# Performance work log

Hardware: AMD Instinct MI355X
Metric: run time of the kernel (lower is better)

## Reference

```python
import jax, jax.numpy as jnp
import numpy as np

H = 32  # hidden size
I = 1   # input size


def setup_inputs() -> dict:
    key = jax.random.key(0)
    ks = jax.random.split(key, 8)
    B, T = 1024, 2048
    s = 1.0 / np.sqrt(H)  # PyTorch default uniform init bound
    u = lambda k, shape: jax.random.uniform(k, shape, jnp.float32, -s, s)
    return {
        "x": jax.random.normal(ks[0], (B, T, I), jnp.float32),
        "W_ih": u(ks[1], (4 * H, I)),   # gate order: i, f, g, o
        "W_hh": u(ks[2], (4 * H, H)),
        "b_ih": u(ks[3], (4 * H,)),
        "b_hh": u(ks[4], (4 * H,)),
        "W_out": u(ks[5], (1, H)),
        "b_out": u(ks[6], (1,)),
    }


def reference(x, W_ih, W_hh, b_ih, b_hh, W_out, b_out):
    B, T, _ = x.shape
    # Precompute input contributions to all gates for all timesteps: [B,T,4H]
    xg = jnp.einsum('bti,gi->btg', x, W_ih) + b_ih + b_hh

    def step(carry, xg_t):
        h, c = carry  # each [B,H]
        gates = xg_t + h @ W_hh.T  # [B,4H]
        i, f, g, o = jnp.split(gates, 4, axis=-1)
        i = jax.nn.sigmoid(i)
        f = jax.nn.sigmoid(f)
        g = jnp.tanh(g)
        o = jax.nn.sigmoid(o)
        c = f * c + i * g
        h = o * jnp.tanh(c)
        return (h, c), h

    h0 = jnp.zeros((B, H), x.dtype)
    c0 = jnp.zeros((B, H), x.dtype)
    _, hs = jax.lax.scan(step, (h0, c0), jnp.swapaxes(xg, 0, 1))  # hs: [T,B,H]
    r_out = jnp.swapaxes(hs, 0, 1)  # [B,T,H]
    # Per-timestep linear (the original Python loop) == one batched matmul
    return jnp.einsum('bth,oh->bto', r_out, W_out) + b_out  # [B,T,1]
```

## Files before the change

kernel.cpp:

```cpp
#include <hip/hip_runtime.h>

#define LOG2E 1.44269504088896340736f

typedef _Float16 half2_t __attribute__((ext_vector_type(2)));

__device__ __forceinline__ float rlf(float v, int lane) {
    return __int_as_float(__builtin_amdgcn_readlane(__float_as_int(v), lane));
}
__device__ __forceinline__ unsigned rlu(unsigned v, int lane) {
    return (unsigned)__builtin_amdgcn_readlane((int)v, lane);
}
__device__ __forceinline__ unsigned pack2(float a, float b) {
    half2_t v; v.x = (_Float16)a; v.y = (_Float16)b;
    return __builtin_bit_cast(unsigned, v);
}
__device__ __forceinline__ half2_t ubc(unsigned u) {
    return __builtin_bit_cast(half2_t, u);
}

__device__ __forceinline__ float swap_half(float v) {
#if __has_builtin(__builtin_amdgcn_permlane32_swap)
    const unsigned u = __builtin_bit_cast(unsigned, v);
    auto r = __builtin_amdgcn_permlane32_swap(u, u, false, false);
    return __builtin_bit_cast(float, (unsigned)(r[0] ^ r[1] ^ u));
#else
    return __shfl_xor(v, 32, 64);
#endif
}

__device__ __forceinline__ float xor1_dpp(float v) {
    return __int_as_float(__builtin_amdgcn_mov_dpp(
        __float_as_int(v), 0xB1, 0xF, 0xF, true));
}

__global__ __launch_bounds__(64, 1) void lstm_pl_kernel(
    const float* __restrict__ x,
    const float* __restrict__ W_ih,
    const float* __restrict__ W_hh,
    const float* __restrict__ b_ih,
    const float* __restrict__ b_hh,
    const float* __restrict__ W_out,
    const float* __restrict__ b_out,
    float* __restrict__ out,
    int T)
{
    __shared__ float psum[64 * 68];
    __shared__ __align__(16) unsigned hbc[80];

    const int b = blockIdx.x;
    const int l = threadIdx.x;
    const int r0 = l;
    const int r1 = l + 64;
    const bool lo = (l < 32);

    const float sc0 = -LOG2E;
    const float sc1 = lo ? (-2.0f * LOG2E) : (-LOG2E);

    unsigned w0u[16], w1u[16];
#pragma unroll
    for (int m = 0; m < 16; ++m) {
        w0u[m] = pack2(W_hh[r0 * 32 + 2 * m] * sc0,
                       W_hh[r0 * 32 + 2 * m + 1] * sc0);
        w1u[m] = pack2(W_hh[r1 * 32 + 2 * m] * sc1,
                       W_hh[r1 * 32 + 2 * m + 1] * sc1);
    }
#pragma unroll
    for (int m = 0; m < 16; ++m)
        asm volatile("" : "+v"(w0u[m]), "+v"(w1u[m]));

    float4 wout4[8];
#pragma unroll
    for (int m = 0; m < 8; ++m)
        wout4[m] = *(const float4*)(W_out + 4 * m);

    const float wih0  = W_ih[r0] * sc0;
    const float wih1  = W_ih[r1] * sc1;
    const float bias0 = (b_ih[r0] + b_hh[r0]) * sc0;
    const float bias1 = (b_ih[r1] + b_hh[r1]) * sc1;
    const float A1s = lo ? (-4.0f * LOG2E) : 1.0f;
    const float B1s = lo ? ( 2.0f * LOG2E) : 0.0f;
    const float bout  = b_out[0];

    const bool pub = lo && !(l & 1) && (l >= 8);
    const int waddr = pub ? (l >> 1) : (16 + l);

    float h = 0.0f, cs = 0.0f;
    unsigned hpk = 0u;
    uint4 hqB = {0,0,0,0}, hqC = {0,0,0,0}, hqD = {0,0,0,0};

    const float* xp = x + (size_t)b * T;
    float*       op = out + (size_t)b * T;
    float xv = xp[l];

    const uint4* hb4 = (const uint4*)hbc;

    for (int t0 = 0; t0 < T; t0 += 64) {
        const int tn = (t0 + 64 < T) ? (t0 + 64) : t0;
        float xv_next = xp[tn + l];

#pragma unroll 16
        for (int tu = 0; tu < 64; ++tu) {
            const float xt = rlf(xv, tu);

            const unsigned hp0 = rlu(hpk, 0);
            const unsigned hp1 = rlu(hpk, 2);
            const unsigned hp2 = rlu(hpk, 4);
            const unsigned hp3 = rlu(hpk, 6);

            float a0 = fmaf(wih0, xt, bias0);
            float a1 = fmaf(wih1, xt, bias1);
            float b0 = 0.0f, b1 = 0.0f;
            a0 = __builtin_amdgcn_fdot2(ubc(w0u[0]),  ubc(hp0),   a0, false);
            b0 = __builtin_amdgcn_fdot2(ubc(w0u[1]),  ubc(hp1),   b0, false);
            a1 = __builtin_amdgcn_fdot2(ubc(w1u[0]),  ubc(hp0),   a1, false);
            b1 = __builtin_amdgcn_fdot2(ubc(w1u[1]),  ubc(hp1),   b1, false);
            a0 = __builtin_amdgcn_fdot2(ubc(w0u[2]),  ubc(hp2),   a0, false);
            b0 = __builtin_amdgcn_fdot2(ubc(w0u[3]),  ubc(hp3),   b0, false);
            a1 = __builtin_amdgcn_fdot2(ubc(w1u[2]),  ubc(hp2),   a1, false);
            b1 = __builtin_amdgcn_fdot2(ubc(w1u[3]),  ubc(hp3),   b1, false);
            a0 = __builtin_amdgcn_fdot2(ubc(w0u[4]),  ubc(hqB.x), a0, false);
            b0 = __builtin_amdgcn_fdot2(ubc(w0u[5]),  ubc(hqB.y), b0, false);
            a1 = __builtin_amdgcn_fdot2(ubc(w1u[4]),  ubc(hqB.x), a1, false);
            b1 = __builtin_amdgcn_fdot2(ubc(w1u[5]),  ubc(hqB.y), b1, false);
            a0 = __builtin_amdgcn_fdot2(ubc(w0u[6]),  ubc(hqB.z), a0, false);
            b0 = __builtin_amdgcn_fdot2(ubc(w0u[7]),  ubc(hqB.w), b0, false);
            a1 = __builtin_amdgcn_fdot2(ubc(w1u[6]),  ubc(hqB.z), a1, false);
            b1 = __builtin_amdgcn_fdot2(ubc(w1u[7]),  ubc(hqB.w), b1, false);
            a0 = __builtin_amdgcn_fdot2(ubc(w0u[8]),  ubc(hqC.x), a0, false);
            b0 = __builtin_amdgcn_fdot2(ubc(w0u[9]),  ubc(hqC.y), b0, false);
            a1 = __builtin_amdgcn_fdot2(ubc(w1u[8]),  ubc(hqC.x), a1, false);
            b1 = __builtin_amdgcn_fdot2(ubc(w1u[9]),  ubc(hqC.y), b1, false);
            a0 = __builtin_amdgcn_fdot2(ubc(w0u[10]), ubc(hqC.z), a0, false);
            b0 = __builtin_amdgcn_fdot2(ubc(w0u[11]), ubc(hqC.w), b0, false);
            a1 = __builtin_amdgcn_fdot2(ubc(w1u[10]), ubc(hqC.z), a1, false);
            b1 = __builtin_amdgcn_fdot2(ubc(w1u[11]), ubc(hqC.w), b1, false);
            a0 = __builtin_amdgcn_fdot2(ubc(w0u[12]), ubc(hqD.x), a0, false);
            b0 = __builtin_amdgcn_fdot2(ubc(w0u[13]), ubc(hqD.y), b0, false);
            a1 = __builtin_amdgcn_fdot2(ubc(w1u[12]), ubc(hqD.x), a1, false);
            b1 = __builtin_amdgcn_fdot2(ubc(w1u[13]), ubc(hqD.y), b1, false);
            a0 = __builtin_amdgcn_fdot2(ubc(w0u[14]), ubc(hqD.z), a0, false);
            b0 = __builtin_amdgcn_fdot2(ubc(w0u[15]), ubc(hqD.w), b0, false);
            a1 = __builtin_amdgcn_fdot2(ubc(w1u[14]), ubc(hqD.z), a1, false);
            b1 = __builtin_amdgcn_fdot2(ubc(w1u[15]), ubc(hqD.w), b1, false);
            const float G0 = a0 + b0;
            const float G1 = a1 + b1;

            const float s0  = __builtin_amdgcn_rcpf(1.0f + __builtin_amdgcn_exp2f(G0));
            const float s1s = fmaf(A1s, __builtin_amdgcn_rcpf(
                                  1.0f + __builtin_amdgcn_exp2f(G1)), B1s);
            const float ig = s0 * s1s;

            const float o0 = swap_half(s0);
            const float o1 = swap_half(s1s);
            const float to1 = o1 + o1;

            cs = fmaf(o0, cs, ig);
            const float rc = __builtin_amdgcn_rcpf(
                1.0f + __builtin_amdgcn_exp2f(cs));
            h = fmaf(to1, rc, -o1);

            const float hn = xor1_dpp(h);
            hpk = __builtin_bit_cast(unsigned,
                      __builtin_amdgcn_cvt_pkrtz(h, hn));
            hbc[waddr] = hpk;
            psum[tu * 68 + l] = h;
            hqB = hb4[1];
            hqC = hb4[2];
            hqD = hb4[3];
        }

        __syncthreads();
        const float4* row = (const float4*)(psum + l * 68);
        float4 s4;
        {
            float4 v4 = row[0];
            s4.x = v4.x * wout4[0].x; s4.y = v4.y * wout4[0].y;
            s4.z = v4.z * wout4[0].z; s4.w = v4.w * wout4[0].w;
        }
#pragma unroll
        for (int m = 1; m < 8; ++m) {
            float4 v4 = row[m];
            s4.x = fmaf(v4.x, wout4[m].x, s4.x);
            s4.y = fmaf(v4.y, wout4[m].y, s4.y);
            s4.z = fmaf(v4.z, wout4[m].z, s4.z);
            s4.w = fmaf(v4.w, wout4[m].w, s4.w);
        }
        op[t0 + l] = (s4.x + s4.y) + (s4.z + s4.w) + bout;
        __syncthreads();
        xv = xv_next;
    }
}

extern "C" void kernel_launch(void* const* d_in, const int* in_sizes, int n_in,
                              void* d_out, int out_size, void* d_ws, size_t ws_size,
                              hipStream_t stream) {
    const float* x     = (const float*)d_in[0];
    const float* W_ih  = (const float*)d_in[1];
    const float* W_hh  = (const float*)d_in[2];
    const float* b_ih  = (const float*)d_in[3];
    const float* b_hh  = (const float*)d_in[4];
    const float* W_out = (const float*)d_in[5];
    const float* b_out = (const float*)d_in[6];
    float* out = (float*)d_out;

    const int B = 1024;
    const int T = 2048;
    lstm_pl_kernel<<<B, 64, 0, stream>>>(x, W_ih, W_hh, b_ih, b_hh,
                                         W_out, b_out, out, T);
}
```

Measured before the change: 428.6 us.

## Process two batch rows per wave with lane-local gates and DPP h exchange

Each 64-lane wave now handles two sequences, one per 32-lane half. Each lane computes all four gates for one hidden unit, so the permlane32 gate swap is gone. The hidden state is broadcast with a permlane16 swap plus a chain of DPP permutes against pre-permuted weights, replacing the readlane and LDS round trip, and x is staged through shared memory. This halves the grid to 512 blocks and removes LDS latency from the recurrence. In exchange each lane issues twice as many fdot2 operations per step and holds four times as many weight registers.

```diff
diff --git a/kernel.cpp b/kernel.cpp
--- a/kernel.cpp
+++ b/kernel.cpp
@@ -4,12 +4,6 @@
 
 typedef _Float16 half2_t __attribute__((ext_vector_type(2)));
 
-__device__ __forceinline__ float rlf(float v, int lane) {
-    return __int_as_float(__builtin_amdgcn_readlane(__float_as_int(v), lane));
-}
-__device__ __forceinline__ unsigned rlu(unsigned v, int lane) {
-    return (unsigned)__builtin_amdgcn_readlane((int)v, lane);
-}
 __device__ __forceinline__ unsigned pack2(float a, float b) {
     half2_t v; v.x = (_Float16)a; v.y = (_Float16)b;
     return __builtin_bit_cast(unsigned, v);
@@ -18,22 +12,21 @@
     return __builtin_bit_cast(half2_t, u);
 }
 
-__device__ __forceinline__ float swap_half(float v) {
-#if __has_builtin(__builtin_amdgcn_permlane32_swap)
-    const unsigned u = __builtin_bit_cast(unsigned, v);
-    auto r = __builtin_amdgcn_permlane32_swap(u, u, false, false);
-    return __builtin_bit_cast(float, (unsigned)(r[0] ^ r[1] ^ u));
+template <int CTRL>
+__device__ __forceinline__ unsigned dppx(unsigned v) {
+    return (unsigned)__builtin_amdgcn_mov_dpp((int)v, CTRL, 0xF, 0xF, true);
+}
+
+__device__ __forceinline__ unsigned lanex16(unsigned u) {
+#if __has_builtin(__builtin_amdgcn_permlane16_swap)
+    auto r = __builtin_amdgcn_permlane16_swap(u, u, false, false);
+    return (unsigned)(r[0] ^ r[1] ^ u);
 #else
-    return __shfl_xor(v, 32, 64);
+    return (unsigned)__builtin_amdgcn_ds_swizzle((int)u, 0x401F);
 #endif
 }
 
-__device__ __forceinline__ float xor1_dpp(float v) {
-    return __int_as_float(__builtin_amdgcn_mov_dpp(
-        __float_as_int(v), 0xB1, 0xF, 0xF, true));
-}
-
-__global__ __launch_bounds__(64, 1) void lstm_pl_kernel(
+__global__ __launch_bounds__(64, 1) void lstm_pl2_kernel(
     const float* __restrict__ x,
     const float* __restrict__ W_ih,
     const float* __restrict__ W_hh,
@@ -44,150 +37,158 @@
     float* __restrict__ out,
     int T)
 {
-    __shared__ float psum[64 * 68];
-    __shared__ __align__(16) unsigned hbc[80];
-
-    const int b = blockIdx.x;
-    const int l = threadIdx.x;
-    const int r0 = l;
-    const int r1 = l + 64;
-    const bool lo = (l < 32);
-
-    const float sc0 = -LOG2E;
-    const float sc1 = lo ? (-2.0f * LOG2E) : (-LOG2E);
-
-    unsigned w0u[16], w1u[16];
-#pragma unroll
-    for (int m = 0; m < 16; ++m) {
-        w0u[m] = pack2(W_hh[r0 * 32 + 2 * m] * sc0,
-                       W_hh[r0 * 32 + 2 * m + 1] * sc0);
-        w1u[m] = pack2(W_hh[r1 * 32 + 2 * m] * sc1,
-                       W_hh[r1 * 32 + 2 * m + 1] * sc1);
+    __shared__ __align__(16) float psum[64 * 68];
+    __shared__ float xs[2 * 72];
+
+    const int b  = blockIdx.x;
+    const int l  = threadIdx.x;
+    const int kl = l & 31;
+    const int hf = l >> 5;
+
+    const float sA = -LOG2E;
+    const float sG = -2.0f * LOG2E;
+
+    const int ri = kl, rf2 = 32 + kl, rg = 64 + kl, ro = 96 + kl;
+
+    const int X[16] = {0,2,5,7,8,10,13,15, 16,18,21,23,24,26,29,31};
+
+    unsigned wi[16], wf[16], wg[16], wo[16];
+#pragma unroll
+    for (int j = 0; j < 16; ++j) {
+        const int xl = kl ^ X[j];
+        const int q2 = xl & ~1;
+        const int s  = xl & 1;
+        wi[j] = pack2(W_hh[ri *32 + q2 + s] * sA, W_hh[ri *32 + q2 + (s^1)] * sA);
+        wf[j] = pack2(W_hh[rf2*32 + q2 + s] * sA, W_hh[rf2*32 + q2 + (s^1)] * sA);
+        wg[j] = pack2(W_hh[rg *32 + q2 + s] * sG, W_hh[rg *32 + q2 + (s^1)] * sG);
+        wo[j] = pack2(W_hh[ro *32 + q2 + s] * sA, W_hh[ro *32 + q2 + (s^1)] * sA);
     }
 #pragma unroll
-    for (int m = 0; m < 16; ++m)
-        asm volatile("" : "+v"(w0u[m]), "+v"(w1u[m]));
+    for (int j = 0; j < 16; ++j)
+        asm volatile("" : "+v"(wi[j]), "+v"(wf[j]), "+v"(wg[j]), "+v"(wo[j]));
 
     float4 wout4[8];
 #pragma unroll
-    for (int m = 0; m < 8; ++m)
-        wout4[m] = *(const float4*)(W_out + 4 * m);
-
-    const float wih0  = W_ih[r0] * sc0;
-    const float wih1  = W_ih[r1] * sc1;
-    const float bias0 = (b_ih[r0] + b_hh[r0]) * sc0;
-    const float bias1 = (b_ih[r1] + b_hh[r1]) * sc1;
-    const float A1s = lo ? (-4.0f * LOG2E) : 1.0f;
-    const float B1s = lo ? ( 2.0f * LOG2E) : 0.0f;
-    const float bout  = b_out[0];
-
-    const bool pub = lo && !(l & 1) && (l >= 8);
-    const int waddr = pub ? (l >> 1) : (16 + l);
+    for (int m = 0; m < 8; ++m) wout4[m] = *(const float4*)(W_out + 4 * m);
+
+    const float wxi = W_ih[ri ] * sA;
+    const float wxf = W_ih[rf2] * sA;
+    const float wxg = W_ih[rg ] * sG;
+    const float wxo = W_ih[ro ] * sA;
+    const float bi_ = (b_ih[ri ] + b_hh[ri ]) * sA;
+    const float bf_ = (b_ih[rf2] + b_hh[rf2]) * sA;
+    const float bg_ = (b_ih[rg ] + b_hh[rg ]) * sG;
+    const float bo_ = (b_ih[ro ] + b_hh[ro ]) * sA;
+    const float bout = b_out[0];
+
+    const float* xpA = x + (size_t)(2*b)     * T;
+    const float* xpB = x + (size_t)(2*b + 1) * T;
+    float*       opA = out + (size_t)(2*b)     * T;
+    float*       opB = out + (size_t)(2*b + 1) * T;
+
+    float* xsh = xs + 72 * hf;
+    const int pcol = kl + 36 * hf;
+
+    xs[l]      = xpA[l];
+    xs[72 + l] = xpB[l];
 
     float h = 0.0f, cs = 0.0f;
     unsigned hpk = 0u;
-    uint4 hqB = {0,0,0,0}, hqC = {0,0,0,0}, hqD = {0,0,0,0};
-
-    const float* xp = x + (size_t)b * T;
-    float*       op = out + (size_t)b * T;
-    float xv = xp[l];
-
-    const uint4* hb4 = (const uint4*)hbc;
 
     for (int t0 = 0; t0 < T; t0 += 64) {
         const int tn = (t0 + 64 < T) ? (t0 + 64) : t0;
-        float xv_next = xp[tn + l];
-
-#pragma unroll 16
+        const float na = xpA[tn + l];
+        const float nb = xpB[tn + l];
+
+        float xt0 = xsh[0], xt1 = xsh[1];
+
+#pragma unroll 8
         for (int tu = 0; tu < 64; ++tu) {
-            const float xt = rlf(xv, tu);
-
-            const unsigned hp0 = rlu(hpk, 0);
-            const unsigned hp1 = rlu(hpk, 2);
-            const unsigned hp2 = rlu(hpk, 4);
-            const unsigned hp3 = rlu(hpk, 6);
-
-            float a0 = fmaf(wih0, xt, bias0);
-            float a1 = fmaf(wih1, xt, bias1);
-            float b0 = 0.0f, b1 = 0.0f;
-            a0 = __builtin_amdgcn_fdot2(ubc(w0u[0]),  ubc(hp0),   a0, false);
-            b0 = __builtin_amdgcn_fdot2(ubc(w0u[1]),  ubc(hp1),   b0, false);
-            a1 = __builtin_amdgcn_fdot2(ubc(w1u[0]),  ubc(hp0),   a1, false);
-            b1 = __builtin_amdgcn_fdot2(ubc(w1u[1]),  ubc(hp1),   b1, false);
-            a0 = __builtin_amdgcn_fdot2(ubc(w0u[2]),  ubc(hp2),   a0, false);
-            b0 = __builtin_amdgcn_fdot2(ubc(w0u[3]),  ubc(hp3),   b0, false);
-            a1 = __builtin_amdgcn_fdot2(ubc(w1u[2]),  ubc(hp2),   a1, false);
-            b1 = __builtin_amdgcn_fdot2(ubc(w1u[3]),  ubc(hp3),   b1, false);
-            a0 = __builtin_amdgcn_fdot2(ubc(w0u[4]),  ubc(hqB.x), a0, false);
-            b0 = __builtin_amdgcn_fdot2(ubc(w0u[5]),  ubc(hqB.y), b0, false);
-            a1 = __builtin_amdgcn_fdot2(ubc(w1u[4]),  ubc(hqB.x), a1, false);
-            b1 = __builtin_amdgcn_fdot2(ubc(w1u[5]),  ubc(hqB.y), b1, false);
-            a0 = __builtin_amdgcn_fdot2(ubc(w0u[6]),  ubc(hqB.z), a0, false);
-            b0 = __builtin_amdgcn_fdot2(ubc(w0u[7]),  ubc(hqB.w), b0, false);
-            a1 = __builtin_amdgcn_fdot2(ubc(w1u[6]),  ubc(hqB.z), a1, false);
-            b1 = __builtin_amdgcn_fdot2(ubc(w1u[7]),  ubc(hqB.w), b1, false);
-            a0 = __builtin_amdgcn_fdot2(ubc(w0u[8]),  ubc(hqC.x), a0, false);
-            b0 = __builtin_amdgcn_fdot2(ubc(w0u[9]),  ubc(hqC.y), b0, false);
-            a1 = __builtin_amdgcn_fdot2(ubc(w1u[8]),  ubc(hqC.x), a1, false);
-            b1 = __builtin_amdgcn_fdot2(ubc(w1u[9]),  ubc(hqC.y), b1, false);
-            a0 = __builtin_amdgcn_fdot2(ubc(w0u[10]), ubc(hqC.z), a0, false);
-            b0 = __builtin_amdgcn_fdot2(ubc(w0u[11]), ubc(hqC.w), b0, false);
-            a1 = __builtin_amdgcn_fdot2(ubc(w1u[10]), ubc(hqC.z), a1, false);
-            b1 = __builtin_amdgcn_fdot2(ubc(w1u[11]), ubc(hqC.w), b1, false);
-            a0 = __builtin_amdgcn_fdot2(ubc(w0u[12]), ubc(hqD.x), a0, false);
-            b0 = __builtin_amdgcn_fdot2(ubc(w0u[13]), ubc(hqD.y), b0, false);
-            a1 = __builtin_amdgcn_fdot2(ubc(w1u[12]), ubc(hqD.x), a1, false);
-            b1 = __builtin_amdgcn_fdot2(ubc(w1u[13]), ubc(hqD.y), b1, false);
-            a0 = __builtin_amdgcn_fdot2(ubc(w0u[14]), ubc(hqD.z), a0, false);
-            b0 = __builtin_amdgcn_fdot2(ubc(w0u[15]), ubc(hqD.w), b0, false);
-            a1 = __builtin_amdgcn_fdot2(ubc(w1u[14]), ubc(hqD.z), a1, false);
-            b1 = __builtin_amdgcn_fdot2(ubc(w1u[15]), ubc(hqD.w), b1, false);
-            const float G0 = a0 + b0;
-            const float G1 = a1 + b1;
-
-            const float s0  = __builtin_amdgcn_rcpf(1.0f + __builtin_amdgcn_exp2f(G0));
-            const float s1s = fmaf(A1s, __builtin_amdgcn_rcpf(
-                                  1.0f + __builtin_amdgcn_exp2f(G1)), B1s);
-            const float ig = s0 * s1s;
-
-            const float o0 = swap_half(s0);
-            const float o1 = swap_half(s1s);
-            const float to1 = o1 + o1;
-
-            cs = fmaf(o0, cs, ig);
-            const float rc = __builtin_amdgcn_rcpf(
-                1.0f + __builtin_amdgcn_exp2f(cs));
-            h = fmaf(to1, rc, -o1);
-
-            const float hn = xor1_dpp(h);
-            hpk = __builtin_bit_cast(unsigned,
-                      __builtin_amdgcn_cvt_pkrtz(h, hn));
-            hbc[waddr] = hpk;
-            psum[tu * 68 + l] = h;
-            hqB = hb4[1];
-            hqC = hb4[2];
-            hqD = hb4[3];
+            const float xt = (tu & 1) ? xt1 : xt0;
+            float GiA = fmaf(wxi, xt, bi_);
+            float GfA = fmaf(wxf, xt, bf_);
+            float GgA = fmaf(wxg, xt, bg_);
+            float GoA = fmaf(wxo, xt, bo_);
+            float GiB = 0.0f, GfB = 0.0f, GgB = 0.0f, GoB = 0.0f;
+
+            unsigned ha = hpk;
+            unsigned hb = lanex16(hpk);
+
+#define DOTS(j, HA, HB) \
+            GiA = __builtin_amdgcn_fdot2(ubc(wi[j]),   ubc(HA), GiA, false); \
+            GfA = __builtin_amdgcn_fdot2(ubc(wf[j]),   ubc(HA), GfA, false); \
+            GgA = __builtin_amdgcn_fdot2(ubc(wg[j]),   ubc(HA), GgA, false); \
+            GoA = __builtin_amdgcn_fdot2(ubc(wo[j]),   ubc(HA), GoA, false); \
+            GiB = __builtin_amdgcn_fdot2(ubc(wi[8+j]), ubc(HB), GiB, false); \
+            GfB = __builtin_amdgcn_fdot2(ubc(wf[8+j]), ubc(HB), GfB, false); \
+            GgB = __builtin_amdgcn_fdot2(ubc(wg[8+j]), ubc(HB), GgB, false); \
+            GoB = __builtin_amdgcn_fdot2(ubc(wo[8+j]), ubc(HB), GoB, false);
+
+            DOTS(0, ha, hb)
+            ha = dppx<0x4E>(ha);  hb = dppx<0x4E>(hb);
+            DOTS(1, ha, hb)
+            ha = dppx<0x141>(ha); hb = dppx<0x141>(hb);
+            DOTS(2, ha, hb)
+            ha = dppx<0x4E>(ha);  hb = dppx<0x4E>(hb);
+            DOTS(3, ha, hb)
+            ha = dppx<0x140>(ha); hb = dppx<0x140>(hb);
+            DOTS(4, ha, hb)
+            ha = dppx<0x4E>(ha);  hb = dppx<0x4E>(hb);
+            DOTS(5, ha, hb)
+            ha = dppx<0x141>(ha); hb = dppx<0x141>(hb);
+            DOTS(6, ha, hb)
+            ha = dppx<0x4E>(ha);  hb = dppx<0x4E>(hb);
+            DOTS(7, ha, hb)
+#undef DOTS
+
+            const float Gi = GiA + GiB;
+            const float Gf = GfA + GfB;
+            const float Gg = GgA + GgB;
+            const float Go = GoA + GoB;
+
+            const float i_ = __builtin_amdgcn_rcpf(1.0f + __builtin_amdgcn_exp2f(Gi));
+            const float f_ = __builtin_amdgcn_rcpf(1.0f + __builtin_amdgcn_exp2f(Gf));
+            const float o_ = __builtin_amdgcn_rcpf(1.0f + __builtin_amdgcn_exp2f(Go));
+            const float gs = fmaf(-4.0f * LOG2E,
+                __builtin_amdgcn_rcpf(1.0f + __builtin_amdgcn_exp2f(Gg)),
+                2.0f * LOG2E);
+
+            cs = fmaf(f_, cs, i_ * gs);
+            const float rc = __builtin_amdgcn_rcpf(1.0f + __builtin_amdgcn_exp2f(cs));
+            h = fmaf(o_ + o_, rc, -o_);
+
+            const float hn = __int_as_float(__builtin_amdgcn_mov_dpp(
+                __float_as_int(h), 0xB1, 0xF, 0xF, true));
+            hpk = __builtin_bit_cast(unsigned, __builtin_amdgcn_cvt_pkrtz(h, hn));
+
+            psum[tu * 68 + pcol] = h;
+            if (!(tu & 1)) xt0 = xsh[tu + 2]; else xt1 = xsh[tu + 2];
         }
 
         __syncthreads();
-        const float4* row = (const float4*)(psum + l * 68);
-        float4 s4;
-        {
-            float4 v4 = row[0];
-            s4.x = v4.x * wout4[0].x; s4.y = v4.y * wout4[0].y;
-            s4.z = v4.z * wout4[0].z; s4.w = v4.w * wout4[0].w;
+#pragma unroll
+        for (int s = 0; s < 2; ++s) {
+            const float4* row = (const float4*)(psum + l * 68 + 36 * s);
+            float4 a4;
+            {
+                float4 v4 = row[0];
+                a4.x = v4.x * wout4[0].x; a4.y = v4.y * wout4[0].y;
+                a4.z = v4.z * wout4[0].z; a4.w = v4.w * wout4[0].w;
+            }
+#pragma unroll
+            for (int m = 1; m < 8; ++m) {
+                float4 v4 = row[m];
+                a4.x = fmaf(v4.x, wout4[m].x, a4.x);
+                a4.y = fmaf(v4.y, wout4[m].y, a4.y);
+                a4.z = fmaf(v4.z, wout4[m].z, a4.z);
+                a4.w = fmaf(v4.w, wout4[m].w, a4.w);
+            }
+            const float r = (a4.x + a4.y) + (a4.z + a4.w) + bout;
+            if (s == 0) opA[t0 + l] = r; else opB[t0 + l] = r;
         }
-#pragma unroll
-        for (int m = 1; m < 8; ++m) {
-            float4 v4 = row[m];
-            s4.x = fmaf(v4.x, wout4[m].x, s4.x);
-            s4.y = fmaf(v4.y, wout4[m].y, s4.y);
-            s4.z = fmaf(v4.z, wout4[m].z, s4.z);
-            s4.w = fmaf(v4.w, wout4[m].w, s4.w);
-        }
-        op[t0 + l] = (s4.x + s4.y) + (s4.z + s4.w) + bout;
         __syncthreads();
-        xv = xv_next;
+        xs[l]      = na;
+        xs[72 + l] = nb;
     }
 }
 
@@ -205,6 +206,6 @@
 
     const int B = 1024;
     const int T = 2048;
-    lstm_pl_kernel<<<B, 64, 0, stream>>>(x, W_ih, W_hh, b_ih, b_hh,
-                                         W_out, b_out, out, T);
-}
+    lstm_pl2_kernel<<<B / 2, 64, 0, stream>>>(x, W_ih, W_hh, b_ih, b_hh,
+                                              W_out, b_out, out, T);
+}
```

Result: slower. 551.7 us (+28.7%).

## Interleave two independent batch sequences per wavefront to hide recurrence latency

Applied to the files above, without the earlier changes.

Each 64-lane block now runs two batch elements' LSTM recurrences interleaved in one instruction stream, and the grid is halved to 512 blocks. The aim is to fill the latency of the serial dependency chain (dot products, exp/rcp, LDS round trips, cross-lane swaps) with independent work from the second sequence. In exchange the per-step instruction count doubles for each wave, register and LDS use roughly double, and with only 512 waves on a 256-CU device the machine may be underfilled, so the single-sequence step latency still sets the critical path.

```diff
diff --git a/kernel.cpp b/kernel.cpp
--- a/kernel.cpp
+++ b/kernel.cpp
@@ -33,7 +33,7 @@
         __float_as_int(v), 0xB1, 0xF, 0xF, true));
 }
 
-__global__ __launch_bounds__(64, 1) void lstm_pl_kernel(
+__global__ __launch_bounds__(64, 1) void lstm_dual_kernel(
     const float* __restrict__ x,
     const float* __restrict__ W_ih,
     const float* __restrict__ W_hh,
@@ -44,8 +44,10 @@
     float* __restrict__ out,
     int T)
 {
-    __shared__ float psum[64 * 68];
-    __shared__ __align__(16) unsigned hbc[80];
+    __shared__ float psumA[64 * 68];
+    __shared__ float psumB[64 * 68];
+    __shared__ __align__(16) unsigned hbcA[80];
+    __shared__ __align__(16) unsigned hbcB[80];
 
     const int b = blockIdx.x;
     const int l = threadIdx.x;
@@ -84,110 +86,152 @@
     const bool pub = lo && !(l & 1) && (l >= 8);
     const int waddr = pub ? (l >> 1) : (16 + l);
 
-    float h = 0.0f, cs = 0.0f;
-    unsigned hpk = 0u;
-    uint4 hqB = {0,0,0,0}, hqC = {0,0,0,0}, hqD = {0,0,0,0};
-
-    const float* xp = x + (size_t)b * T;
-    float*       op = out + (size_t)b * T;
-    float xv = xp[l];
-
-    const uint4* hb4 = (const uint4*)hbc;
+    float hA = 0.0f, csA = 0.0f;
+    float hB = 0.0f, csB = 0.0f;
+    unsigned hpkA = 0u, hpkB = 0u;
+    uint4 hqAB = {0,0,0,0}, hqAC = {0,0,0,0}, hqAD = {0,0,0,0};
+    uint4 hqBB = {0,0,0,0}, hqBC = {0,0,0,0}, hqBD = {0,0,0,0};
+
+    const float* xpA = x + (size_t)(2 * b)     * T;
+    const float* xpB = x + (size_t)(2 * b + 1) * T;
+    float*       opA = out + (size_t)(2 * b)     * T;
+    float*       opB = out + (size_t)(2 * b + 1) * T;
+    float xvA = xpA[l];
+    float xvB = xpB[l];
+
+    const uint4* hb4A = (const uint4*)hbcA;
+    const uint4* hb4B = (const uint4*)hbcB;
 
     for (int t0 = 0; t0 < T; t0 += 64) {
         const int tn = (t0 + 64 < T) ? (t0 + 64) : t0;
-        float xv_next = xp[tn + l];
-
-#pragma unroll 16
+        float nA = xpA[tn + l];
+        float nB = xpB[tn + l];
+
+#pragma unroll 8
         for (int tu = 0; tu < 64; ++tu) {
-            const float xt = rlf(xv, tu);
-
-            const unsigned hp0 = rlu(hpk, 0);
-            const unsigned hp1 = rlu(hpk, 2);
-            const unsigned hp2 = rlu(hpk, 4);
-            const unsigned hp3 = rlu(hpk, 6);
-
-            float a0 = fmaf(wih0, xt, bias0);
-            float a1 = fmaf(wih1, xt, bias1);
-            float b0 = 0.0f, b1 = 0.0f;
-            a0 = __builtin_amdgcn_fdot2(ubc(w0u[0]),  ubc(hp0),   a0, false);
-            b0 = __builtin_amdgcn_fdot2(ubc(w0u[1]),  ubc(hp1),   b0, false);
-            a1 = __builtin_amdgcn_fdot2(ubc(w1u[0]),  ubc(hp0),   a1, false);
-            b1 = __builtin_amdgcn_fdot2(ubc(w1u[1]),  ubc(hp1),   b1, false);
-            a0 = __builtin_amdgcn_fdot2(ubc(w0u[2]),  ubc(hp2),   a0, false);
-            b0 = __builtin_amdgcn_fdot2(ubc(w0u[3]),  ubc(hp3),   b0, false);
-            a1 = __builtin_amdgcn_fdot2(ubc(w1u[2]),  ubc(hp2),   a1, false);
-            b1 = __builtin_amdgcn_fdot2(ubc(w1u[3]),  ubc(hp3),   b1, false);
-            a0 = __builtin_amdgcn_fdot2(ubc(w0u[4]),  ubc(hqB.x), a0, false);
-            b0 = __builtin_amdgcn_fdot2(ubc(w0u[5]),  ubc(hqB.y), b0, false);
-            a1 = __builtin_amdgcn_fdot2(ubc(w1u[4]),  ubc(hqB.x), a1, false);
-            b1 = __builtin_amdgcn_fdot2(ubc(w1u[5]),  ubc(hqB.y), b1, false);
-            a0 = __builtin_amdgcn_fdot2(ubc(w0u[6]),  ubc(hqB.z), a0, false);
-            b0 = __builtin_amdgcn_fdot2(ubc(w0u[7]),  ubc(hqB.w), b0, false);
-            a1 = __builtin_amdgcn_fdot2(ubc(w1u[6]),  ubc(hqB.z), a1, false);
-            b1 = __builtin_amdgcn_fdot2(ubc(w1u[7]),  ubc(hqB.w), b1, false);
-            a0 = __builtin_amdgcn_fdot2(ubc(w0u[8]),  ubc(hqC.x), a0, false);
-            b0 = __builtin_amdgcn_fdot2(ubc(w0u[9]),  ubc(hqC.y), b0, false);
-            a1 = __builtin_amdgcn_fdot2(ubc(w1u[8]),  ubc(hqC.x), a1, false);
-            b1 = __builtin_amdgcn_fdot2(ubc(w1u[9]),  ubc(hqC.y), b1, false);
-            a0 = __builtin_amdgcn_fdot2(ubc(w0u[10]), ubc(hqC.z), a0, false);
-            b0 = __builtin_amdgcn_fdot2(ubc(w0u[11]), ubc(hqC.w), b0, false);
-            a1 = __builtin_amdgcn_fdot2(ubc(w1u[10]), ubc(hqC.z), a1, false);
-            b1 = __builtin_amdgcn_fdot2(ubc(w1u[11]), ubc(hqC.w), b1, false);
-            a0 = __builtin_amdgcn_fdot2(ubc(w0u[12]), ubc(hqD.x), a0, false);
-            b0 = __builtin_amdgcn_fdot2(ubc(w0u[13]), ubc(hqD.y), b0, false);
-            a1 = __builtin_amdgcn_fdot2(ubc(w1u[12]), ubc(hqD.x), a1, false);
-            b1 = __builtin_amdgcn_fdot2(ubc(w1u[13]), ubc(hqD.y), b1, false);
-            a0 = __builtin_amdgcn_fdot2(ubc(w0u[14]), ubc(hqD.z), a0, false);
-            b0 = __builtin_amdgcn_fdot2(ubc(w0u[15]), ubc(hqD.w), b0, false);
-            a1 = __builtin_amdgcn_fdot2(ubc(w1u[14]), ubc(hqD.z), a1, false);
-            b1 = __builtin_amdgcn_fdot2(ubc(w1u[15]), ubc(hqD.w), b1, false);
-            const float G0 = a0 + b0;
-            const float G1 = a1 + b1;
-
-            const float s0  = __builtin_amdgcn_rcpf(1.0f + __builtin_amdgcn_exp2f(G0));
-            const float s1s = fmaf(A1s, __builtin_amdgcn_rcpf(
-                                  1.0f + __builtin_amdgcn_exp2f(G1)), B1s);
-            const float ig = s0 * s1s;
-
-            const float o0 = swap_half(s0);
-            const float o1 = swap_half(s1s);
-            const float to1 = o1 + o1;
-
-            cs = fmaf(o0, cs, ig);
-            const float rc = __builtin_amdgcn_rcpf(
-                1.0f + __builtin_amdgcn_exp2f(cs));
-            h = fmaf(to1, rc, -o1);
-
-            const float hn = xor1_dpp(h);
-            hpk = __builtin_bit_cast(unsigned,
-                      __builtin_amdgcn_cvt_pkrtz(h, hn));
-            hbc[waddr] = hpk;
-            psum[tu * 68 + l] = h;
-            hqB = hb4[1];
-            hqC = hb4[2];
-            hqD = hb4[3];
+            const float xtA = rlf(xvA, tu);
+            const float xtB = rlf(xvB, tu);
+
+            const unsigned hA0 = rlu(hpkA, 0), hA1 = rlu(hpkA, 2);
+            const unsigned hA2 = rlu(hpkA, 4), hA3 = rlu(hpkA, 6);
+            const unsigned hB0 = rlu(hpkB, 0), hB1 = rlu(hpkB, 2);
+            const unsigned hB2 = rlu(hpkB, 4), hB3 = rlu(hpkB, 6);
+
+            float a0A = fmaf(wih0, xtA, bias0);
+            float a1A = fmaf(wih1, xtA, bias1);
+            float b0A = 0.0f, b1A = 0.0f;
+            float a0B = fmaf(wih0, xtB, bias0);
+            float a1B = fmaf(wih1, xtB, bias1);
+            float b0B = 0.0f, b1B = 0.0f;
+
+#define FD(acc, w, h) acc = __builtin_amdgcn_fdot2(ubc(w), ubc(h), acc, false)
+            FD(a0A, w0u[0], hA0);  FD(b0A, w0u[1], hA1);
+            FD(a1A, w1u[0], hA0);  FD(b1A, w1u[1], hA1);
+            FD(a0B, w0u[0], hB0);  FD(b0B, w0u[1], hB1);
+            FD(a1B, w1u[0], hB0);  FD(b1B, w1u[1], hB1);
+            FD(a0A, w0u[2], hA2);  FD(b0A, w0u[3], hA3);
+            FD(a1A, w1u[2], hA2);  FD(b1A, w1u[3], hA3);
+            FD(a0B, w0u[2], hB2);  FD(b0B, w0u[3], hB3);
+            FD(a1B, w1u[2], hB2);  FD(b1B, w1u[3], hB3);
+            FD(a0A, w0u[4],  hqAB.x);  FD(b0A, w0u[5],  hqAB.y);
+            FD(a1A, w1u[4],  hqAB.x);  FD(b1A, w1u[5],  hqAB.y);
+            FD(a0A, w0u[6],  hqAB.z);  FD(b0A, w0u[7],  hqAB.w);
+            FD(a1A, w1u[6],  hqAB.z);  FD(b1A, w1u[7],  hqAB.w);
+            FD(a0A, w0u[8],  hqAC.x);  FD(b0A, w0u[9],  hqAC.y);
+            FD(a1A, w1u[8],  hqAC.x);  FD(b1A, w1u[9],  hqAC.y);
+            FD(a0A, w0u[10], hqAC.z);  FD(b0A, w0u[11], hqAC.w);
+            FD(a1A, w1u[10], hqAC.z);  FD(b1A, w1u[11], hqAC.w);
+            FD(a0A, w0u[12], hqAD.x);  FD(b0A, w0u[13], hqAD.y);
+            FD(a1A, w1u[12], hqAD.x);  FD(b1A, w1u[13], hqAD.y);
+            FD(a0A, w0u[14], hqAD.z);  FD(b0A, w0u[15], hqAD.w);
+            FD(a1A, w1u[14], hqAD.z);  FD(b1A, w1u[15], hqAD.w);
+            FD(a0B, w0u[4],  hqBB.x);  FD(b0B, w0u[5],  hqBB.y);
+            FD(a1B, w1u[4],  hqBB.x);  FD(b1B, w1u[5],  hqBB.y);
+            FD(a0B, w0u[6],  hqBB.z);  FD(b0B, w0u[7],  hqBB.w);
+            FD(a1B, w1u[6],  hqBB.z);  FD(b1B, w1u[7],  hqBB.w);
+            FD(a0B, w0u[8],  hqBC.x);  FD(b0B, w0u[9],  hqBC.y);
+            FD(a1B, w1u[8],  hqBC.x);  FD(b1B, w1u[9],  hqBC.y);
+            FD(a0B, w0u[10], hqBC.z);  FD(b0B, w0u[11], hqBC.w);
+            FD(a1B, w1u[10], hqBC.z);  FD(b1B, w1u[11], hqBC.w);
+            FD(a0B, w0u[12], hqBD.x);  FD(b0B, w0u[13], hqBD.y);
+            FD(a1B, w1u[12], hqBD.x);  FD(b1B, w1u[13], hqBD.y);
+            FD(a0B, w0u[14], hqBD.z);  FD(b0B, w0u[15], hqBD.w);
+            FD(a1B, w1u[14], hqBD.z);  FD(b1B, w1u[15], hqBD.w);
+#undef FD
+
+            const float GA0 = a0A + b0A;
+            const float GA1 = a1A + b1A;
+            const float GB0 = a0B + b0B;
+            const float GB1 = a1B + b1B;
+
+            const float s0A  = __builtin_amdgcn_rcpf(1.0f + __builtin_amdgcn_exp2f(GA0));
+            const float s0B  = __builtin_amdgcn_rcpf(1.0f + __builtin_amdgcn_exp2f(GB0));
+            const float s1sA = fmaf(A1s, __builtin_amdgcn_rcpf(
+                                   1.0f + __builtin_amdgcn_exp2f(GA1)), B1s);
+            const float s1sB = fmaf(A1s, __builtin_amdgcn_rcpf(
+                                   1.0f + __builtin_amdgcn_exp2f(GB1)), B1s);
+            const float igA = s0A * s1sA;
+            const float igB = s0B * s1sB;
+
+            const float o0A = swap_half(s0A);
+            const float o1A = swap_half(s1sA);
+            const float o0B = swap_half(s0B);
+            const float o1B = swap_half(s1sB);
+            const float to1A = o1A + o1A;
+            const float to1B = o1B + o1B;
+
+            csA = fmaf(o0A, csA, igA);
+            csB = fmaf(o0B, csB, igB);
+            const float rcA = __builtin_amdgcn_rcpf(
+                1.0f + __builtin_amdgcn_exp2f(csA));
+            const float rcB = __builtin_amdgcn_rcpf(
+                1.0f + __builtin_amdgcn_exp2f(csB));
+            hA = fmaf(to1A, rcA, -o1A);
+            hB = fmaf(to1B, rcB, -o1B);
+
+            const float hnA = xor1_dpp(hA);
+            const float hnB = xor1_dpp(hB);
+            hpkA = __builtin_bit_cast(unsigned,
+                       __builtin_amdgcn_cvt_pkrtz(hA, hnA));
+            hpkB = __builtin_bit_cast(unsigned,
+                       __builtin_amdgcn_cvt_pkrtz(hB, hnB));
+            hbcA[waddr] = hpkA;
+            hbcB[waddr] = hpkB;
+            psumA[tu * 68 + l] = hA;
+            psumB[tu * 68 + l] = hB;
+            hqAB = hb4A[1];
+            hqAC = hb4A[2];
+            hqAD = hb4A[3];
+            hqBB = hb4B[1];
+            hqBC = hb4B[2];
+            hqBD = hb4B[3];
         }
 
         __syncthreads();
-        const float4* row = (const float4*)(psum + l * 68);
-        float4 s4;
-        {
-            float4 v4 = row[0];
-            s4.x = v4.x * wout4[0].x; s4.y = v4.y * wout4[0].y;
-            s4.z = v4.z * wout4[0].z; s4.w = v4.w * wout4[0].w;
+#pragma unroll
+        for (int s = 0; s < 2; ++s) {
+            const float* ps = (s == 0) ? psumA : psumB;
+            const float4* row = (const float4*)(ps + l * 68);
+            float4 s4;
+            {
+                float4 v4 = row[0];
+                s4.x = v4.x * wout4[0].x; s4.y = v4.y * wout4[0].y;
+                s4.z = v4.z * wout4[0].z; s4.w = v4.w * wout4[0].w;
+            }
+#pragma unroll
+            for (int m = 1; m < 8; ++m) {
+                float4 v4 = row[m];
+                s4.x = fmaf(v4.x, wout4[m].x, s4.x);
+                s4.y = fmaf(v4.y, wout4[m].y, s4.y);
+                s4.z = fmaf(v4.z, wout4[m].z, s4.z);
+                s4.w = fmaf(v4.w, wout4[m].w, s4.w);
+            }
+            const float r = (s4.x + s4.y) + (s4.z + s4.w) + bout;
+            if (s == 0) opA[t0 + l] = r; else opB[t0 + l] = r;
         }
-#pragma unroll
-        for (int m = 1; m < 8; ++m) {
-            float4 v4 = row[m];
-            s4.x = fmaf(v4.x, wout4[m].x, s4.x);
-            s4.y = fmaf(v4.y, wout4[m].y, s4.y);
-            s4.z = fmaf(v4.z, wout4[m].z, s4.z);
-            s4.w = fmaf(v4.w, wout4[m].w, s4.w);
-        }
-        op[t0 + l] = (s4.x + s4.y) + (s4.z + s4.w) + bout;
         __syncthreads();
-        xv = xv_next;
+        xvA = nA;
+        xvB = nB;
     }
 }
 
@@ -205,6 +249,6 @@
 
     const int B = 1024;
     const int T = 2048;
-    lstm_pl_kernel<<<B, 64, 0, stream>>>(x, W_ih, W_hh, b_ih, b_hh,
-                                         W_out, b_out, out, T);
-}
+    lstm_dual_kernel<<<B / 2, 64, 0, stream>>>(x, W_ih, W_hh, b_ih, b_hh,
+                                               W_out, b_out, out, T);
+}
```

Result: slower. 708.7 us (+65.4%).
